# Kernel tuning notes

Measured on AMD Instinct MI355X. Metric: run time of the kernel, lower is better.

Reference implementation:

```python
import jax, jax.numpy as jnp
import numpy as np

N = 500_000   # total nodes
B = 4096      # number of graphs (segments)
D = 256       # feature dim (input_dim)
H = 4         # attention heads


def setup_inputs() -> dict:
    key = jax.random.key(0)
    ks = jax.random.split(key, 9)
    x = jax.random.normal(ks[0], (N, D), dtype=jnp.float32)
    membership = jnp.sort(jax.random.randint(ks[1], (N,), 0, B, dtype=jnp.int32))
    # xavier-normal-ish attention weight, shape (1, H, D//H)
    att_w = jax.random.normal(ks[2], (1, H, D // H), dtype=jnp.float32) * np.float32(np.sqrt(2.0 / (1 + D // H)))
    s = np.float32(1.0 / np.sqrt(D))
    gru_w_ih = jax.random.uniform(ks[3], (3 * D, D), minval=-s, maxval=s, dtype=jnp.float32)
    gru_w_hh = jax.random.uniform(ks[4], (3 * D, D), minval=-s, maxval=s, dtype=jnp.float32)
    gru_b_ih = jax.random.uniform(ks[5], (3 * D,), minval=-s, maxval=s, dtype=jnp.float32)
    gru_b_hh = jax.random.uniform(ks[6], (3 * D,), minval=-s, maxval=s, dtype=jnp.float32)
    sm = np.float32(1.0 / np.sqrt(4 * D))
    merge_w = jax.random.uniform(ks[7], (D, 4 * D), minval=-sm, maxval=sm, dtype=jnp.float32)
    merge_b = jax.random.uniform(ks[8], (D,), minval=-sm, maxval=sm, dtype=jnp.float32)
    return {"x": x, "membership": membership, "att_w": att_w,
            "gru_w_ih": gru_w_ih, "gru_w_hh": gru_w_hh,
            "gru_b_ih": gru_b_ih, "gru_b_hh": gru_b_hh,
            "merge_w": merge_w, "merge_b": merge_b}


def _readout(x, seg, att_w, gru_w_ih, gru_w_hh, gru_b_ih, gru_b_hh, merge_w, merge_b):
    n, d = x.shape
    # ---- branch 0: 'rnn-sum-max' (GRUCell on pseudo-nodes) ----
    h = jax.nn.gelu(x, approximate=False)                       # exact gelu as torch F.gelu
    center = jax.ops.segment_sum(h, seg, num_segments=B)        # op_center = 'sum'  (B, D)
    neighbor = jax.ops.segment_max(h, seg, num_segments=B)      # op_neighbor = 'max' (B, D)
    gi = center @ gru_w_ih.T + gru_b_ih                          # (B, 3D)
    gh = neighbor @ gru_w_hh.T + gru_b_hh                        # (B, 3D)
    i_r, i_z, i_n = jnp.split(gi, 3, axis=-1)
    h_r, h_z, h_n = jnp.split(gh, 3, axis=-1)
    r = jax.nn.sigmoid(i_r + h_r)
    z = jax.nn.sigmoid(i_z + h_z)
    ng = jnp.tanh(i_n + r * h_n)
    rnn_out = (1.0 - z) * ng + z * neighbor                      # (B, D)
    # ---- branch 1: 'att' (single mode, segment softmax) ----
    xv = x.reshape(n, H, d // H)
    alpha = jax.nn.leaky_relu(jnp.sum(xv * att_w, axis=-1), negative_slope=0.2)  # (N, H)
    amax = jax.ops.segment_max(alpha, seg, num_segments=B)       # (B, H)
    e = jnp.exp(alpha - amax[seg])
    denom = jax.ops.segment_sum(e, seg, num_segments=B)
    a = e / denom[seg]                                           # segment softmax (N, H)
    att_out = jax.ops.segment_sum((xv * a[:, :, None]).reshape(n, d), seg, num_segments=B)
    # ---- branch 2/3: 'max', 'sum' ----
    max_out = jax.ops.segment_max(x, seg, num_segments=B)
    sum_out = jax.ops.segment_sum(x, seg, num_segments=B)
    # ---- merge: cat + Linear ----
    merged = jnp.concatenate([rnn_out, att_out, max_out, sum_out], axis=-1)  # (B, 4D)
    return merged @ merge_w.T + merge_b                          # (B, D)


def reference(x, membership, att_w, gru_w_ih, gru_w_hh, gru_b_ih, gru_b_hh, merge_w, merge_b):
    return _readout(x, membership, att_w, gru_w_ih, gru_w_hh, gru_b_ih, gru_b_hh, merge_w, merge_b)
```

## Files before the change

kernel.cpp:

```cpp
#include <hip/hip_runtime.h>
#include <math.h>
#include <stdint.h>

#define NN 500000
#define NB 4096
#define DD 256

typedef short  short8  __attribute__((ext_vector_type(8)));
typedef short  short4v __attribute__((ext_vector_type(4)));
typedef float  floatx4 __attribute__((ext_vector_type(4)));
typedef float  f2      __attribute__((ext_vector_type(2)));

__device__ __forceinline__ f2 sp(float v) { return (f2){v, v}; }

__device__ __forceinline__ short f2bf(float f) {
    uint32_t u = __float_as_uint(f);
    u += 0x7fffu + ((u >> 16) & 1u);
    return (short)(u >> 16);
}
__device__ __forceinline__ float bf2f(short s) {
    uint32_t u = ((uint32_t)(unsigned short)s) << 16;
    return __uint_as_float(u);
}

__device__ __forceinline__ f2 gelu2(f2 x) {
    f2 z = __builtin_elementwise_abs(x) * sp(0.70710678118654752440f);
    f2 p = __builtin_elementwise_fma(z, sp(0.0000430638f), sp(0.0002765672f));
    p = __builtin_elementwise_fma(p, z, sp(0.0001520143f));
    p = __builtin_elementwise_fma(p, z, sp(0.0092705272f));
    p = __builtin_elementwise_fma(p, z, sp(0.0422820123f));
    p = __builtin_elementwise_fma(p, z, sp(0.0705230784f));
    p = __builtin_elementwise_fma(p, z, sp(1.0f));
    p = p * p; p = p * p; p = p * p; p = p * p;
    f2 r = { __builtin_amdgcn_rcpf(p.x), __builtin_amdgcn_rcpf(p.y) };
    f2 er = __builtin_elementwise_copysign(sp(1.0f) - r, x);
    return sp(0.5f) * x * (sp(1.0f) + er);
}

__global__ __launch_bounds__(256) void seg_bounds(
    const int* __restrict__ seg, int* __restrict__ bnd)
{
    int i = blockIdx.x * 256 + threadIdx.x;
    if (i >= NN) return;
    int s = seg[i];
    if (i == 0) {
        for (int b = 0; b <= s; ++b) bnd[b] = 0;
    } else {
        int p = seg[i - 1];
        for (int b = p + 1; b <= s; ++b) bnd[b] = i;
    }
    if (i == NN - 1) {
        for (int b = s + 1; b <= NB; ++b) bnd[b] = NN;
    }
}

__global__ __launch_bounds__(256, 8) void seg_kernel(
    const float* __restrict__ x,
    const int*   __restrict__ bnd,
    const float* __restrict__ att_w,
    short* __restrict__ merged_bf,
    short* __restrict__ center_bf,
    short* __restrict__ neighbor_bf)
{
    const int b   = blockIdx.x;
    const int tid = threadIdx.x;
    const int w   = tid >> 6;
    const int l   = tid & 63;

    const int start = bnd[b];
    const int end   = bnd[b + 1];

    const int cnt = end - start;
    const int q = cnt >> 2, r = cnt & 3;
    const int my_start = start + w * q + (w < r ? w : r);
    const int my_cnt   = q + (w < r ? 1 : 0);

    const float4 awv = *reinterpret_cast<const float4*>(&att_w[4 * l]);
    const f2 aw01 = {awv.x, awv.y}, aw23 = {awv.z, awv.w};

    f2 c01 = sp(0.f), c23 = sp(0.f);
    f2 s01 = sp(0.f), s23 = sp(0.f);
    f2 m01 = sp(-INFINITY), m23 = sp(-INFINITY);
    f2 a01 = sp(0.f), a23 = sp(0.f);
    float lsum = 0.f;

    auto process = [&](const float4& v) {
        f2 vl = {v.x, v.y}, vh = {v.z, v.w};
        f2 gl = gelu2(vl), gh = gelu2(vh);
        c01 += gl; c23 += gh;
        s01 += vl; s23 += vh;
        m01 = __builtin_elementwise_max(m01, vl);
        m23 = __builtin_elementwise_max(m23, vh);
        f2 tp = __builtin_elementwise_fma(vh, aw23, vl * aw01);
        float t = tp.x + tp.y;
        t += __shfl_xor(t, 1, 64);
        t += __shfl_xor(t, 2, 64);
        t += __shfl_xor(t, 4, 64);
        t += __shfl_xor(t, 8, 64);
        float alpha = fmaxf(t, 0.2f * t);
        float e = __expf(alpha);
        lsum += e;
        f2 ev = sp(e);
        a01 = __builtin_elementwise_fma(ev, vl, a01);
        a23 = __builtin_elementwise_fma(ev, vh, a23);
    };

    const float* __restrict__ xl = x + 4 * l;
    auto LD = [&](int row) -> float4 {
        int rc = row < (NN - 1) ? row : (NN - 1);
        return *reinterpret_cast<const float4*>(&xl[(size_t)rc * DD]);
    };

    float4 q0 = LD(my_start),     q1 = LD(my_start + 1),
           q2 = LD(my_start + 2), q3 = LD(my_start + 3);
    int ip = my_start + 4;
    int rem = my_cnt;
    while (rem >= 2) {
        float4 f0 = LD(ip), f1 = LD(ip + 1);
        process(q0); process(q1);
        q0 = q2; q1 = q3; q2 = f0; q3 = f1;
        ip += 2; rem -= 2;
    }
    if (rem) process(q0);

    __shared__ float lds[4][4][256];
    __shared__ float ldsl[4][4];
    const int c = 4 * l;
    lds[0][w][c+0] = c01.x; lds[0][w][c+1] = c01.y; lds[0][w][c+2] = c23.x; lds[0][w][c+3] = c23.y;
    lds[1][w][c+0] = s01.x; lds[1][w][c+1] = s01.y; lds[1][w][c+2] = s23.x; lds[1][w][c+3] = s23.y;
    lds[2][w][c+0] = m01.x; lds[2][w][c+1] = m01.y; lds[2][w][c+2] = m23.x; lds[2][w][c+3] = m23.y;
    lds[3][w][c+0] = a01.x; lds[3][w][c+1] = a01.y; lds[3][w][c+2] = a23.x; lds[3][w][c+3] = a23.y;
    if ((l & 15) == 0) ldsl[w][l >> 4] = lsum;
    __syncthreads();

    const int d = tid;
    float cs = lds[0][0][d] + lds[0][1][d] + lds[0][2][d] + lds[0][3][d];
    float ss = lds[1][0][d] + lds[1][1][d] + lds[1][2][d] + lds[1][3][d];
    float mm = fmaxf(fmaxf(lds[2][0][d], lds[2][1][d]), fmaxf(lds[2][2][d], lds[2][3][d]));
    float ac = lds[3][0][d] + lds[3][1][d] + lds[3][2][d] + lds[3][3][d];
    const int h = d >> 6;
    float denom = ldsl[0][h] + ldsl[1][h] + ldsl[2][h] + ldsl[3][h];
    float att = (denom > 0.f) ? ac / denom : 0.f;
    float nm = gelu2((f2){mm, mm}).x;

    short* mrow = merged_bf + (size_t)b * 1024;
    mrow[256 + d] = f2bf(att);
    mrow[512 + d] = f2bf(mm);
    mrow[768 + d] = f2bf(ss);
    center_bf  [(size_t)b * DD + d] = f2bf(cs);
    neighbor_bf[(size_t)b * DD + d] = f2bf(nm);
}

__global__ __launch_bounds__(256) void gemm_gru(
    const short* __restrict__ center_bf,
    const short* __restrict__ neighbor_bf,
    const float* __restrict__ w_ih,
    const float* __restrict__ w_hh,
    const float* __restrict__ b_ih,
    const float* __restrict__ b_hh,
    short* __restrict__ merged_bf)
{
    __shared__ short Ac[64 * 72];
    __shared__ short An[64 * 72];
    __shared__ short Wt[6][16 * 72];

    const int t   = threadIdx.x;
    const int w   = t >> 6, l = t & 63;
    const int m0  = blockIdx.x * 64;
    const int j0  = blockIdx.y * 16;
    const int lr  = t >> 2;
    const int lc  = (t & 3) * 16;
    const int l15 = l & 15, lq = l >> 4;

    int wg[6], wrow[6], wk4[6];
    const float* wbase[6];
    #pragma unroll
    for (int i = 0; i < 6; ++i) {
        int f = i * 256 + t;
        wg[i] = f >> 8;
        int idx = f & 255;
        wrow[i] = idx >> 4;
        wk4[i]  = (idx & 15) * 4;
        wbase[i] = (wg[i] < 3)
            ? &w_ih[(size_t)(wg[i] * 256 + j0 + wrow[i]) * 256 + wk4[i]]
            : &w_hh[(size_t)((wg[i] - 3) * 256 + j0 + wrow[i]) * 256 + wk4[i]];
    }
    const short* crp = &center_bf  [(size_t)(m0 + lr) * 256 + lc];
    const short* nrp = &neighbor_bf[(size_t)(m0 + lr) * 256 + lc];

    floatx4 acc[6] = {};

    short8 c0 = *(const short8*)(crp), c1 = *(const short8*)(crp + 8);
    short8 n0 = *(const short8*)(nrp), n1 = *(const short8*)(nrp + 8);
    float4 wv[6];
    #pragma unroll
    for (int i = 0; i < 6; ++i) wv[i] = *(const float4*)(wbase[i]);

    for (int k0 = 0; k0 < 256; k0 += 64) {
        const int kn = (k0 + 64 < 256) ? k0 + 64 : k0;
        short8 nc0 = *(const short8*)(crp + kn), nc1 = *(const short8*)(crp + kn + 8);
        short8 nn0 = *(const short8*)(nrp + kn), nn1 = *(const short8*)(nrp + kn + 8);
        float4 nwv[6];
        #pragma unroll
        for (int i = 0; i < 6; ++i) nwv[i] = *(const float4*)(wbase[i] + kn);

        short4v w4[6];
        #pragma unroll
        for (int i = 0; i < 6; ++i)
            w4[i] = (short4v){ f2bf(wv[i].x), f2bf(wv[i].y), f2bf(wv[i].z), f2bf(wv[i].w) };

        __syncthreads();
        *(short8*)&Ac[lr * 72 + lc]     = c0;
        *(short8*)&Ac[lr * 72 + lc + 8] = c1;
        *(short8*)&An[lr * 72 + lc]     = n0;
        *(short8*)&An[lr * 72 + lc + 8] = n1;
        #pragma unroll
        for (int i = 0; i < 6; ++i)
            *(short4v*)&Wt[wg[i]][wrow[i] * 72 + wk4[i]] = w4[i];
        __syncthreads();

        short8 afc[2], afn[2];
        #pragma unroll
        for (int ks = 0; ks < 2; ++ks) {
            afc[ks] = *(short8*)&Ac[(w * 16 + l15) * 72 + ks * 32 + lq * 8];
            afn[ks] = *(short8*)&An[(w * 16 + l15) * 72 + ks * 32 + lq * 8];
        }
        #pragma unroll
        for (int gg = 0; gg < 6; ++gg) {
            #pragma unroll
            for (int ks = 0; ks < 2; ++ks) {
                short8 bf = *(short8*)&Wt[gg][l15 * 72 + ks * 32 + lq * 8];
                acc[gg] = __builtin_amdgcn_mfma_f32_16x16x32_bf16(
                    (gg < 3) ? afc[ks] : afn[ks], bf, acc[gg], 0, 0, 0);
            }
        }

        c0 = nc0; c1 = nc1; n0 = nn0; n1 = nn1;
        #pragma unroll
        for (int i = 0; i < 6; ++i) wv[i] = nwv[i];
    }

    const int col = j0 + l15;
    const float bir = b_ih[col], biz = b_ih[256 + col], bin = b_ih[512 + col];
    const float bhr = b_hh[col], bhz = b_hh[256 + col], bhn = b_hh[512 + col];
    #pragma unroll
    for (int qq = 0; qq < 4; ++qq) {
        const int row = m0 + w * 16 + lq * 4 + qq;
        float rr = 1.f / (1.f + __expf(-(acc[0][qq] + bir + acc[3][qq] + bhr)));
        float zz = 1.f / (1.f + __expf(-(acc[1][qq] + biz + acc[4][qq] + bhz)));
        float ng = tanhf(acc[2][qq] + bin + rr * (acc[5][qq] + bhn));
        float nb = bf2f(neighbor_bf[(size_t)row * 256 + col]);
        merged_bf[(size_t)row * 1024 + col] = f2bf((1.f - zz) * ng + zz * nb);
    }
}

__global__ __launch_bounds__(256) void gemm_bf16(
    const short* __restrict__ A,
    const float* __restrict__ W,
    const float* __restrict__ bias,
    float* __restrict__ C, int K, int ldc)
{
    __shared__ short As[64 * 72];
    __shared__ short Bs[64 * 72];

    const int t   = threadIdx.x;
    const int w   = t >> 6, l = t & 63;
    const int wm  = w >> 1, wn = w & 1;
    const int m0  = blockIdx.x * 64, n0 = blockIdx.y * 64;
    const int arow = t >> 2, ak = (t & 3) * 16;
    const int brow = t >> 2, bkf = (t & 3) * 16;
    const int l15 = l & 15, lq = l >> 4;

    const short* ap = &A[(size_t)(m0 + arow) * K + ak];
    const float* bp = &W[(size_t)(n0 + brow) * K + bkf];

    floatx4 acc[2][2] = {};

    short8 a0 = *(const short8*)(ap), a1 = *(const short8*)(ap + 8);
    float4 b0 = *(const float4*)(bp),      b1 = *(const float4*)(bp + 4);
    float4 b2 = *(const float4*)(bp + 8),  b3 = *(const float4*)(bp + 12);

    for (int k0 = 0; k0 < K; k0 += 64) {
        const int kn = (k0 + 64 < K) ? k0 + 64 : k0;
        short8 na0 = *(const short8*)(ap + kn), na1 = *(const short8*)(ap + kn + 8);
        float4 nb0 = *(const float4*)(bp + kn),      nb1 = *(const float4*)(bp + kn + 4);
        float4 nb2 = *(const float4*)(bp + kn + 8),  nb3 = *(const float4*)(bp + kn + 12);

        short8 w80 = { f2bf(b0.x), f2bf(b0.y), f2bf(b0.z), f2bf(b0.w),
                       f2bf(b1.x), f2bf(b1.y), f2bf(b1.z), f2bf(b1.w) };
        short8 w81 = { f2bf(b2.x), f2bf(b2.y), f2bf(b2.z), f2bf(b2.w),
                       f2bf(b3.x), f2bf(b3.y), f2bf(b3.z), f2bf(b3.w) };

        __syncthreads();
        *(short8*)&As[arow * 72 + ak]      = a0;
        *(short8*)&As[arow * 72 + ak + 8]  = a1;
        *(short8*)&Bs[brow * 72 + bkf]     = w80;
        *(short8*)&Bs[brow * 72 + bkf + 8] = w81;
        __syncthreads();

        #pragma unroll
        for (int ks = 0; ks < 2; ++ks) {
            short8 af0 = *(short8*)&As[(wm * 32 +      l15) * 72 + ks * 32 + lq * 8];
            short8 af1 = *(short8*)&As[(wm * 32 + 16 + l15) * 72 + ks * 32 + lq * 8];
            short8 bf0 = *(short8*)&Bs[(wn * 32 +      l15) * 72 + ks * 32 + lq * 8];
            short8 bf1 = *(short8*)&Bs[(wn * 32 + 16 + l15) * 72 + ks * 32 + lq * 8];
            acc[0][0] = __builtin_amdgcn_mfma_f32_16x16x32_bf16(af0, bf0, acc[0][0], 0, 0, 0);
            acc[0][1] = __builtin_amdgcn_mfma_f32_16x16x32_bf16(af0, bf1, acc[0][1], 0, 0, 0);
            acc[1][0] = __builtin_amdgcn_mfma_f32_16x16x32_bf16(af1, bf0, acc[1][0], 0, 0, 0);
            acc[1][1] = __builtin_amdgcn_mfma_f32_16x16x32_bf16(af1, bf1, acc[1][1], 0, 0, 0);
        }

        a0 = na0; a1 = na1; b0 = nb0; b1 = nb1; b2 = nb2; b3 = nb3;
    }

    #pragma unroll
    for (int mi = 0; mi < 2; ++mi) {
        #pragma unroll
        for (int nj = 0; nj < 2; ++nj) {
            const int col = n0 + wn * 32 + 16 * nj + l15;
            const float bv = bias[col];
            #pragma unroll
            for (int qq = 0; qq < 4; ++qq) {
                const int row = m0 + wm * 32 + 16 * mi + lq * 4 + qq;
                C[(size_t)row * ldc + col] = acc[mi][nj][qq] + bv;
            }
        }
    }
}

extern "C" void kernel_launch(void* const* d_in, const int* in_sizes, int n_in,
                              void* d_out, int out_size, void* d_ws, size_t ws_size,
                              hipStream_t stream) {
    const float* x       = (const float*)d_in[0];
    const int*   seg     = (const int*)  d_in[1];
    const float* att_w   = (const float*)d_in[2];
    const float* w_ih    = (const float*)d_in[3];
    const float* w_hh    = (const float*)d_in[4];
    const float* b_ih    = (const float*)d_in[5];
    const float* b_hh    = (const float*)d_in[6];
    const float* merge_w = (const float*)d_in[7];
    const float* merge_b = (const float*)d_in[8];
    float* out = (float*)d_out;

    short* merged_bf   = (short*)d_ws;
    short* center_bf   = merged_bf   + (size_t)NB * 1024;
    short* neighbor_bf = center_bf   + (size_t)NB * DD;
    int*   bnd         = (int*)(neighbor_bf + (size_t)NB * DD);

    seg_bounds<<<(NN + 255) / 256, 256, 0, stream>>>(seg, bnd);

    seg_kernel<<<NB, 256, 0, stream>>>(x, bnd, att_w, merged_bf, center_bf, neighbor_bf);

    dim3 gg(NB / 64, DD / 16);
    gemm_gru<<<gg, 256, 0, stream>>>(center_bf, neighbor_bf, w_ih, w_hh, b_ih, b_hh, merged_bf);

    dim3 g2(NB / 64, DD / 64);
    gemm_bf16<<<g2, 256, 0, stream>>>(merged_bf, merge_w, merge_b, out, 1024, DD);
}
```

Measured before the change: 140.2 us.

## Pre-convert weights to bf16 and overlap GRU GEMM with partial merge GEMM

The fp32 GRU and merge weights are now converted to bf16 once, inside the segment-bounds kernel, so the GEMM inner loops load half the bytes and skip repeated conversions. The GRU GEMM and the merge GEMM over the att/max/sum columns (K=768) run as separate block ranges of a single launch. A small final kernel then adds the rnn_out contribution (K=256) into the output. This cuts the serial dependency on the GRU result, at the cost of an extra launch and a read-modify-write of the output.

```diff
diff --git a/kernel.cpp b/kernel.cpp
--- a/kernel.cpp
+++ b/kernel.cpp
@@ -5,6 +5,8 @@
 #define NN 500000
 #define NB 4096
 #define DD 256
+#define NBND 1954
+#define WPREP 640
 
 typedef short  short8  __attribute__((ext_vector_type(8)));
 typedef short  short4v __attribute__((ext_vector_type(4)));
@@ -37,20 +39,39 @@
     return sp(0.5f) * x * (sp(1.0f) + er);
 }
 
-__global__ __launch_bounds__(256) void seg_bounds(
-    const int* __restrict__ seg, int* __restrict__ bnd)
+__global__ __launch_bounds__(256) void prep_kernel(
+    const int*   __restrict__ seg,
+    const float* __restrict__ w_ih,
+    const float* __restrict__ w_hh,
+    const float* __restrict__ merge_w,
+    int*   __restrict__ bnd,
+    short* __restrict__ wih_bf,
+    short* __restrict__ whh_bf,
+    short* __restrict__ mw_bf)
 {
-    int i = blockIdx.x * 256 + threadIdx.x;
-    if (i >= NN) return;
-    int s = seg[i];
-    if (i == 0) {
-        for (int b = 0; b <= s; ++b) bnd[b] = 0;
+    const int bid = blockIdx.x;
+    const int t   = threadIdx.x;
+    if (bid < NBND) {
+        int i = bid * 256 + t;
+        if (i >= NN) return;
+        int s = seg[i];
+        if (i == 0) {
+            for (int b = 0; b <= s; ++b) bnd[b] = 0;
+        } else {
+            int p = seg[i - 1];
+            for (int b = p + 1; b <= s; ++b) bnd[b] = i;
+        }
+        if (i == NN - 1) {
+            for (int b = s + 1; b <= NB; ++b) bnd[b] = NN;
+        }
     } else {
-        int p = seg[i - 1];
-        for (int b = p + 1; b <= s; ++b) bnd[b] = i;
-    }
-    if (i == NN - 1) {
-        for (int b = s + 1; b <= NB; ++b) bnd[b] = NN;
+        int base = (bid - NBND) * 1024 + t * 4;
+        const float* src; short* dst;
+        if (base < 196608)      { src = &w_ih[base];            dst = &wih_bf[base]; }
+        else if (base < 393216) { src = &w_hh[base - 196608];   dst = &whh_bf[base - 196608]; }
+        else                    { src = &merge_w[base - 393216]; dst = &mw_bf[base - 393216]; }
+        float4 v = *(const float4*)src;
+        *(short4v*)dst = (short4v){ f2bf(v.x), f2bf(v.y), f2bf(v.z), f2bf(v.w) };
     }
 }
 
@@ -151,114 +172,171 @@
     neighbor_bf[(size_t)b * DD + d] = f2bf(nm);
 }
 
-__global__ __launch_bounds__(256) void gemm_gru(
+__global__ __launch_bounds__(256) void gru_and_basemerge(
     const short* __restrict__ center_bf,
     const short* __restrict__ neighbor_bf,
-    const float* __restrict__ w_ih,
-    const float* __restrict__ w_hh,
+    const short* __restrict__ wih_bf,
+    const short* __restrict__ whh_bf,
     const float* __restrict__ b_ih,
     const float* __restrict__ b_hh,
-    short* __restrict__ merged_bf)
+    short* __restrict__ merged_bf,
+    const short* __restrict__ mw_bf,
+    const float* __restrict__ merge_b,
+    float* __restrict__ out)
 {
-    __shared__ short Ac[64 * 72];
-    __shared__ short An[64 * 72];
-    __shared__ short Wt[6][16 * 72];
-
+    __shared__ short smem[16128];
     const int t   = threadIdx.x;
     const int w   = t >> 6, l = t & 63;
-    const int m0  = blockIdx.x * 64;
-    const int j0  = blockIdx.y * 16;
-    const int lr  = t >> 2;
-    const int lc  = (t & 3) * 16;
     const int l15 = l & 15, lq = l >> 4;
 
-    int wg[6], wrow[6], wk4[6];
-    const float* wbase[6];
-    #pragma unroll
-    for (int i = 0; i < 6; ++i) {
-        int f = i * 256 + t;
-        wg[i] = f >> 8;
-        int idx = f & 255;
-        wrow[i] = idx >> 4;
-        wk4[i]  = (idx & 15) * 4;
-        wbase[i] = (wg[i] < 3)
-            ? &w_ih[(size_t)(wg[i] * 256 + j0 + wrow[i]) * 256 + wk4[i]]
-            : &w_hh[(size_t)((wg[i] - 3) * 256 + j0 + wrow[i]) * 256 + wk4[i]];
-    }
-    const short* crp = &center_bf  [(size_t)(m0 + lr) * 256 + lc];
-    const short* nrp = &neighbor_bf[(size_t)(m0 + lr) * 256 + lc];
-
-    floatx4 acc[6] = {};
-
-    short8 c0 = *(const short8*)(crp), c1 = *(const short8*)(crp + 8);
-    short8 n0 = *(const short8*)(nrp), n1 = *(const short8*)(nrp + 8);
-    float4 wv[6];
-    #pragma unroll
-    for (int i = 0; i < 6; ++i) wv[i] = *(const float4*)(wbase[i]);
-
-    for (int k0 = 0; k0 < 256; k0 += 64) {
-        const int kn = (k0 + 64 < 256) ? k0 + 64 : k0;
-        short8 nc0 = *(const short8*)(crp + kn), nc1 = *(const short8*)(crp + kn + 8);
-        short8 nn0 = *(const short8*)(nrp + kn), nn1 = *(const short8*)(nrp + kn + 8);
-        float4 nwv[6];
+    if (blockIdx.x < 1024) {
+        short* Ac = smem;
+        short* An = smem + 4608;
+        short* Wt = smem + 9216;
+
+        const int m0 = (blockIdx.x >> 4) * 64;
+        const int j0 = (blockIdx.x & 15) * 16;
+        const int lr = t >> 2;
+        const int lc = (t & 3) * 16;
+
+        int wg[3], wrow[3], wk8[3];
+        const short* wbase[3];
         #pragma unroll
-        for (int i = 0; i < 6; ++i) nwv[i] = *(const float4*)(wbase[i] + kn);
-
-        short4v w4[6];
-        #pragma unroll
-        for (int i = 0; i < 6; ++i)
-            w4[i] = (short4v){ f2bf(wv[i].x), f2bf(wv[i].y), f2bf(wv[i].z), f2bf(wv[i].w) };
-
-        __syncthreads();
-        *(short8*)&Ac[lr * 72 + lc]     = c0;
-        *(short8*)&Ac[lr * 72 + lc + 8] = c1;
-        *(short8*)&An[lr * 72 + lc]     = n0;
-        *(short8*)&An[lr * 72 + lc + 8] = n1;
-        #pragma unroll
-        for (int i = 0; i < 6; ++i)
-            *(short4v*)&Wt[wg[i]][wrow[i] * 72 + wk4[i]] = w4[i];
-        __syncthreads();
-
-        short8 afc[2], afn[2];
-        #pragma unroll
-        for (int ks = 0; ks < 2; ++ks) {
-            afc[ks] = *(short8*)&Ac[(w * 16 + l15) * 72 + ks * 32 + lq * 8];
-            afn[ks] = *(short8*)&An[(w * 16 + l15) * 72 + ks * 32 + lq * 8];
-        }
-        #pragma unroll
-        for (int gg = 0; gg < 6; ++gg) {
+        for (int i = 0; i < 3; ++i) {
+            int f = i * 256 + t;
+            wg[i]  = f >> 7;
+            int idx = f & 127;
+            wrow[i] = idx >> 3;
+            wk8[i]  = (idx & 7) * 8;
+            wbase[i] = (wg[i] < 3)
+                ? &wih_bf[(size_t)(wg[i] * 256 + j0 + wrow[i]) * 256 + wk8[i]]
+                : &whh_bf[(size_t)((wg[i] - 3) * 256 + j0 + wrow[i]) * 256 + wk8[i]];
+        }
+        const short* crp = &center_bf  [(size_t)(m0 + lr) * 256 + lc];
+        const short* nrp = &neighbor_bf[(size_t)(m0 + lr) * 256 + lc];
+
+        floatx4 acc[6] = {};
+
+        short8 c0 = *(const short8*)(crp), c1 = *(const short8*)(crp + 8);
+        short8 n0 = *(const short8*)(nrp), n1 = *(const short8*)(nrp + 8);
+        short8 wv0 = *(const short8*)(wbase[0]);
+        short8 wv1 = *(const short8*)(wbase[1]);
+        short8 wv2 = *(const short8*)(wbase[2]);
+
+        for (int k0 = 0; k0 < 256; k0 += 64) {
+            const int kn = (k0 + 64 < 256) ? k0 + 64 : k0;
+            short8 nc0 = *(const short8*)(crp + kn), nc1 = *(const short8*)(crp + kn + 8);
+            short8 nn0 = *(const short8*)(nrp + kn), nn1 = *(const short8*)(nrp + kn + 8);
+            short8 nw0 = *(const short8*)(wbase[0] + kn);
+            short8 nw1 = *(const short8*)(wbase[1] + kn);
+            short8 nw2 = *(const short8*)(wbase[2] + kn);
+
+            __syncthreads();
+            *(short8*)&Ac[lr * 72 + lc]     = c0;
+            *(short8*)&Ac[lr * 72 + lc + 8] = c1;
+            *(short8*)&An[lr * 72 + lc]     = n0;
+            *(short8*)&An[lr * 72 + lc + 8] = n1;
+            *(short8*)&Wt[wg[0] * 1152 + wrow[0] * 72 + wk8[0]] = wv0;
+            *(short8*)&Wt[wg[1] * 1152 + wrow[1] * 72 + wk8[1]] = wv1;
+            *(short8*)&Wt[wg[2] * 1152 + wrow[2] * 72 + wk8[2]] = wv2;
+            __syncthreads();
+
+            short8 afc[2], afn[2];
             #pragma unroll
             for (int ks = 0; ks < 2; ++ks) {
-                short8 bf = *(short8*)&Wt[gg][l15 * 72 + ks * 32 + lq * 8];
-                acc[gg] = __builtin_amdgcn_mfma_f32_16x16x32_bf16(
-                    (gg < 3) ? afc[ks] : afn[ks], bf, acc[gg], 0, 0, 0);
+                afc[ks] = *(short8*)&Ac[(w * 16 + l15) * 72 + ks * 32 + lq * 8];
+                afn[ks] = *(short8*)&An[(w * 16 + l15) * 72 + ks * 32 + lq * 8];
             }
-        }
-
-        c0 = nc0; c1 = nc1; n0 = nn0; n1 = nn1;
+            #pragma unroll
+            for (int gg = 0; gg < 6; ++gg) {
+                #pragma unroll
+                for (int ks = 0; ks < 2; ++ks) {
+                    short8 bf = *(short8*)&Wt[gg * 1152 + l15 * 72 + ks * 32 + lq * 8];
+                    acc[gg] = __builtin_amdgcn_mfma_f32_16x16x32_bf16(
+                        (gg < 3) ? afc[ks] : afn[ks], bf, acc[gg], 0, 0, 0);
+                }
+            }
+
+            c0 = nc0; c1 = nc1; n0 = nn0; n1 = nn1;
+            wv0 = nw0; wv1 = nw1; wv2 = nw2;
+        }
+
+        const int col = j0 + l15;
+        const float bir = b_ih[col], biz = b_ih[256 + col], bin = b_ih[512 + col];
+        const float bhr = b_hh[col], bhz = b_hh[256 + col], bhn = b_hh[512 + col];
         #pragma unroll
-        for (int i = 0; i < 6; ++i) wv[i] = nwv[i];
+        for (int qq = 0; qq < 4; ++qq) {
+            const int row = m0 + w * 16 + lq * 4 + qq;
+            float rr = 1.f / (1.f + __expf(-(acc[0][qq] + bir + acc[3][qq] + bhr)));
+            float zz = 1.f / (1.f + __expf(-(acc[1][qq] + biz + acc[4][qq] + bhz)));
+            float ng = tanhf(acc[2][qq] + bin + rr * (acc[5][qq] + bhn));
+            float nb = bf2f(neighbor_bf[(size_t)row * 256 + col]);
+            merged_bf[(size_t)row * 1024 + col] = f2bf((1.f - zz) * ng + zz * nb);
+        }
+    } else {
+        short* As = smem;
+        short* Bs = smem + 4608;
+
+        const int bid2 = blockIdx.x - 1024;
+        const int m0 = (bid2 & 63) * 64, n0 = (bid2 >> 6) * 64;
+        const int arow = t >> 2, ak = (t & 3) * 16;
+        const int wm = w >> 1, wn = w & 1;
+
+        const short* ap = &merged_bf[(size_t)(m0 + arow) * 1024 + 256 + ak];
+        const short* bp = &mw_bf    [(size_t)(n0 + arow) * 1024 + 256 + ak];
+
+        floatx4 acc[2][2] = {};
+
+        short8 a0 = *(const short8*)(ap), a1 = *(const short8*)(ap + 8);
+        short8 b0 = *(const short8*)(bp), b1 = *(const short8*)(bp + 8);
+
+        for (int k0 = 0; k0 < 768; k0 += 64) {
+            const int kn = (k0 + 64 < 768) ? k0 + 64 : k0;
+            short8 na0 = *(const short8*)(ap + kn), na1 = *(const short8*)(ap + kn + 8);
+            short8 nb0 = *(const short8*)(bp + kn), nb1 = *(const short8*)(bp + kn + 8);
+
+            __syncthreads();
+            *(short8*)&As[arow * 72 + ak]     = a0;
+            *(short8*)&As[arow * 72 + ak + 8] = a1;
+            *(short8*)&Bs[arow * 72 + ak]     = b0;
+            *(short8*)&Bs[arow * 72 + ak + 8] = b1;
+            __syncthreads();
+
+            #pragma unroll
+            for (int ks = 0; ks < 2; ++ks) {
+                short8 af0 = *(short8*)&As[(wm * 32 +      l15) * 72 + ks * 32 + lq * 8];
+                short8 af1 = *(short8*)&As[(wm * 32 + 16 + l15) * 72 + ks * 32 + lq * 8];
+                short8 bf0 = *(short8*)&Bs[(wn * 32 +      l15) * 72 + ks * 32 + lq * 8];
+                short8 bf1 = *(short8*)&Bs[(wn * 32 + 16 + l15) * 72 + ks * 32 + lq * 8];
+                acc[0][0] = __builtin_amdgcn_mfma_f32_16x16x32_bf16(af0, bf0, acc[0][0], 0, 0, 0);
+                acc[0][1] = __builtin_amdgcn_mfma_f32_16x16x32_bf16(af0, bf1, acc[0][1], 0, 0, 0);
+                acc[1][0] = __builtin_amdgcn_mfma_f32_16x16x32_bf16(af1, bf0, acc[1][0], 0, 0, 0);
+                acc[1][1] = __builtin_amdgcn_mfma_f32_16x16x32_bf16(af1, bf1, acc[1][1], 0, 0, 0);
+            }
+
+            a0 = na0; a1 = na1; b0 = nb0; b1 = nb1;
+        }
+
+        #pragma unroll
+        for (int mi = 0; mi < 2; ++mi) {
+            #pragma unroll
+            for (int nj = 0; nj < 2; ++nj) {
+                const int col = n0 + wn * 32 + 16 * nj + l15;
+                const float bv = merge_b[col];
+                #pragma unroll
+                for (int qq = 0; qq < 4; ++qq) {
+                    const int row = m0 + wm * 32 + 16 * mi + lq * 4 + qq;
+                    out[(size_t)row * 256 + col] = acc[mi][nj][qq] + bv;
+                }
+            }
+        }
     }
-
-    const int col = j0 + l15;
-    const float bir = b_ih[col], biz = b_ih[256 + col], bin = b_ih[512 + col];
-    const float bhr = b_hh[col], bhz = b_hh[256 + col], bhn = b_hh[512 + col];
-    #pragma unroll
-    for (int qq = 0; qq < 4; ++qq) {
-        const int row = m0 + w * 16 + lq * 4 + qq;
-        float rr = 1.f / (1.f + __expf(-(acc[0][qq] + bir + acc[3][qq] + bhr)));
-        float zz = 1.f / (1.f + __expf(-(acc[1][qq] + biz + acc[4][qq] + bhz)));
-        float ng = tanhf(acc[2][qq] + bin + rr * (acc[5][qq] + bhn));
-        float nb = bf2f(neighbor_bf[(size_t)row * 256 + col]);
-        merged_bf[(size_t)row * 1024 + col] = f2bf((1.f - zz) * ng + zz * nb);
-    }
-}
-
-__global__ __launch_bounds__(256) void gemm_bf16(
-    const short* __restrict__ A,
-    const float* __restrict__ W,
-    const float* __restrict__ bias,
-    float* __restrict__ C, int K, int ldc)
+}
+
+__global__ __launch_bounds__(256) void rnn_merge(
+    const short* __restrict__ merged_bf,
+    const short* __restrict__ mw_bf,
+    float* __restrict__ out)
 {
     __shared__ short As[64 * 72];
     __shared__ short Bs[64 * 72];
@@ -266,36 +344,28 @@
     const int t   = threadIdx.x;
     const int w   = t >> 6, l = t & 63;
     const int wm  = w >> 1, wn = w & 1;
-    const int m0  = blockIdx.x * 64, n0 = blockIdx.y * 64;
+    const int m0  = (blockIdx.x & 63) * 64, n0 = (blockIdx.x >> 6) * 64;
     const int arow = t >> 2, ak = (t & 3) * 16;
-    const int brow = t >> 2, bkf = (t & 3) * 16;
     const int l15 = l & 15, lq = l >> 4;
 
-    const short* ap = &A[(size_t)(m0 + arow) * K + ak];
-    const float* bp = &W[(size_t)(n0 + brow) * K + bkf];
+    const short* ap = &merged_bf[(size_t)(m0 + arow) * 1024 + ak];
+    const short* bp = &mw_bf    [(size_t)(n0 + arow) * 1024 + ak];
 
     floatx4 acc[2][2] = {};
 
     short8 a0 = *(const short8*)(ap), a1 = *(const short8*)(ap + 8);
-    float4 b0 = *(const float4*)(bp),      b1 = *(const float4*)(bp + 4);
-    float4 b2 = *(const float4*)(bp + 8),  b3 = *(const float4*)(bp + 12);
-
-    for (int k0 = 0; k0 < K; k0 += 64) {
-        const int kn = (k0 + 64 < K) ? k0 + 64 : k0;
+    short8 b0 = *(const short8*)(bp), b1 = *(const short8*)(bp + 8);
+
+    for (int k0 = 0; k0 < 256; k0 += 64) {
+        const int kn = (k0 + 64 < 256) ? k0 + 64 : k0;
         short8 na0 = *(const short8*)(ap + kn), na1 = *(const short8*)(ap + kn + 8);
-        float4 nb0 = *(const float4*)(bp + kn),      nb1 = *(const float4*)(bp + kn + 4);
-        float4 nb2 = *(const float4*)(bp + kn + 8),  nb3 = *(const float4*)(bp + kn + 12);
-
-        short8 w80 = { f2bf(b0.x), f2bf(b0.y), f2bf(b0.z), f2bf(b0.w),
-                       f2bf(b1.x), f2bf(b1.y), f2bf(b1.z), f2bf(b1.w) };
-        short8 w81 = { f2bf(b2.x), f2bf(b2.y), f2bf(b2.z), f2bf(b2.w),
-                       f2bf(b3.x), f2bf(b3.y), f2bf(b3.z), f2bf(b3.w) };
+        short8 nb0 = *(const short8*)(bp + kn), nb1 = *(const short8*)(bp + kn + 8);
 
         __syncthreads();
-        *(short8*)&As[arow * 72 + ak]      = a0;
-        *(short8*)&As[arow * 72 + ak + 8]  = a1;
-        *(short8*)&Bs[brow * 72 + bkf]     = w80;
-        *(short8*)&Bs[brow * 72 + bkf + 8] = w81;
+        *(short8*)&As[arow * 72 + ak]     = a0;
+        *(short8*)&As[arow * 72 + ak + 8] = a1;
+        *(short8*)&Bs[arow * 72 + ak]     = b0;
+        *(short8*)&Bs[arow * 72 + ak + 8] = b1;
         __syncthreads();
 
         #pragma unroll
@@ -310,7 +380,7 @@
             acc[1][1] = __builtin_amdgcn_mfma_f32_16x16x32_bf16(af1, bf1, acc[1][1], 0, 0, 0);
         }
 
-        a0 = na0; a1 = na1; b0 = nb0; b1 = nb1; b2 = nb2; b3 = nb3;
+        a0 = na0; a1 = na1; b0 = nb0; b1 = nb1;
     }
 
     #pragma unroll
@@ -318,11 +388,10 @@
         #pragma unroll
         for (int nj = 0; nj < 2; ++nj) {
             const int col = n0 + wn * 32 + 16 * nj + l15;
-            const float bv = bias[col];
             #pragma unroll
             for (int qq = 0; qq < 4; ++qq) {
                 const int row = m0 + wm * 32 + 16 * mi + lq * 4 + qq;
-                C[(size_t)row * ldc + col] = acc[mi][nj][qq] + bv;
+                out[(size_t)row * 256 + col] += acc[mi][nj][qq];
             }
         }
     }
@@ -346,14 +415,18 @@
     short* center_bf   = merged_bf   + (size_t)NB * 1024;
     short* neighbor_bf = center_bf   + (size_t)NB * DD;
     int*   bnd         = (int*)(neighbor_bf + (size_t)NB * DD);
-
-    seg_bounds<<<(NN + 255) / 256, 256, 0, stream>>>(seg, bnd);
+    short* wih_bf      = (short*)(bnd + 8192);
+    short* whh_bf      = wih_bf + 196608;
+    short* mw_bf       = whh_bf + 196608;
+
+    prep_kernel<<<NBND + WPREP, 256, 0, stream>>>(
+        seg, w_ih, w_hh, merge_w, bnd, wih_bf, whh_bf, mw_bf);
 
     seg_kernel<<<NB, 256, 0, stream>>>(x, bnd, att_w, merged_bf, center_bf, neighbor_bf);
 
-    dim3 gg(NB / 64, DD / 16);
-    gemm_gru<<<gg, 256, 0, stream>>>(center_bf, neighbor_bf, w_ih, w_hh, b_ih, b_hh, merged_bf);
-
-    dim3 g2(NB / 64, DD / 64);
-    gemm_bf16<<<g2, 256, 0, stream>>>(merged_bf, merge_w, merge_b, out, 1024, DD);
-}
+    gru_and_basemerge<<<1024 + 256, 256, 0, stream>>>(
+        center_bf, neighbor_bf, wih_bf, whh_bf, b_ih, b_hh,
+        merged_bf, mw_bf, merge_b, out);
+
+    rnn_merge<<<256, 256, 0, stream>>>(merged_bf, mw_bf, out);
+}
```

Result: faster. 135.0 us (-3.7%).
